# Performance work log

Measured on AMD Instinct MI355X. Metric: run time of the kernel, lower is better.

The kernel has to match this reference:

```python
import jax, jax.numpy as jnp
import numpy as np
from jax import lax

B, L, DIM = 2, 2048, 2048
HK, HV = 16, 32
DK, DV = 128, 128
KCONV = 4
KEY_DIM = HK * DK          # 2048
VAL_DIM = HV * DV          # 4096
CONV_DIM = 2 * KEY_DIM + VAL_DIM  # 8192
EPS = 1e-6


def _l2norm(x, eps=1e-6):
    return x * lax.rsqrt((x * x).sum(-1, keepdims=True) + eps)


def _gated_delta_rule(q, k, v, g, beta):
    # q,k: (B,L,H,DK); v: (B,L,H,DV); g,beta: (B,L,H)
    q = _l2norm(q.astype(jnp.float32)) * (DK ** -0.5)
    k = _l2norm(k.astype(jnp.float32))
    v = v.astype(jnp.float32)
    g = g.astype(jnp.float32)
    beta = beta.astype(jnp.float32)
    # time-major for scan: (L,B,H,...)
    qs = q.transpose(1, 0, 2, 3)
    ks = k.transpose(1, 0, 2, 3)
    vs = v.transpose(1, 0, 2, 3)
    gs = g.transpose(1, 0, 2)
    bs = beta.transpose(1, 0, 2)
    state0 = jnp.zeros((B, HV, DK, DV), jnp.float32)

    def step(state, inp):
        q_t, k_t, v_t, g_t, b_t = inp
        state = state * jnp.exp(g_t)[..., None, None]          # decay
        kv_mem = jnp.einsum('bhk,bhkv->bhv', k_t, state)       # read
        delta = (v_t - kv_mem) * b_t[..., None]                # error-correct
        state = state + jnp.einsum('bhk,bhv->bhkv', k_t, delta)
        out_t = jnp.einsum('bhk,bhkv->bhv', q_t, state)
        return state, out_t

    _, outs = lax.scan(step, state0, (qs, ks, vs, gs, bs))
    return outs.transpose(1, 0, 2, 3)  # (B,L,H,DV)


def setup_inputs() -> dict:
    key = jax.random.key(0)
    ks = jax.random.split(key, 8)
    s = 0.02
    return {
        'x': jax.random.normal(ks[0], (B, L, DIM), jnp.float32),
        'W_qkv': jax.random.normal(ks[1], (CONV_DIM, DIM), jnp.float32) * s,
        'W_z': jax.random.normal(ks[2], (VAL_DIM, DIM), jnp.float32) * s,
        'W_a': jax.random.normal(ks[3], (HV, DIM), jnp.float32) * s,
        'W_b': jax.random.normal(ks[4], (HV, DIM), jnp.float32) * s,
        'conv_w': jax.random.normal(ks[5], (CONV_DIM, 1, KCONV), jnp.float32) * 0.2,
        'A_log': jnp.log(jax.random.uniform(ks[6], (HV,), jnp.float32, 1e-6, 16.0)),
        'dt_bias': jnp.ones((HV,), jnp.float32),
        'norm_weight': jnp.ones((DV,), jnp.float32),
        'W_out': jax.random.normal(ks[7], (DIM, VAL_DIM), jnp.float32) * s,
    }


def reference(x, W_qkv, W_z, W_a, W_b, conv_w, A_log, dt_bias, norm_weight, W_out):
    qkv = x @ W_qkv.T                      # (B,L,CONV_DIM)
    z = x @ W_z.T                          # (B,L,VAL_DIM)
    a = x @ W_a.T                          # (B,L,HV)
    b = x @ W_b.T                          # (B,L,HV)
    # depthwise causal conv1d (left pad K-1)
    h = qkv.transpose(0, 2, 1)             # (B,C,L)
    h = lax.conv_general_dilated(h, conv_w, window_strides=(1,),
                                 padding=[(KCONV - 1, 0)],
                                 dimension_numbers=('NCH', 'OIH', 'NCH'),
                                 feature_group_count=CONV_DIM)
    qkv = jax.nn.silu(h.transpose(0, 2, 1))
    q, k, v = jnp.split(qkv, [KEY_DIM, 2 * KEY_DIM], axis=-1)
    q = q.reshape(B, L, HK, DK)
    k = k.reshape(B, L, HK, DK)
    v = v.reshape(B, L, HV, DV)
    rep = HV // HK
    if rep > 1:
        q = jnp.repeat(q, rep, axis=2)
        k = jnp.repeat(k, rep, axis=2)
    g = -jnp.exp(A_log.astype(jnp.float32)) * jax.nn.softplus(a.astype(jnp.float32) + dt_bias)
    beta = jax.nn.sigmoid(b)
    out = _gated_delta_rule(q, k, v, g, beta)   # (B,L,HV,DV) fp32
    # gated RMSNorm over DV: silu(z) * weight * norm(out)
    var = (out * out).mean(-1, keepdims=True)
    out = out * lax.rsqrt(var + EPS) * norm_weight
    zg = z.reshape(B, L, HV, DV)
    out = out * jax.nn.silu(zg.astype(jnp.float32))
    out = out.astype(x.dtype).reshape(B, L, VAL_DIM)
    return out @ W_out.T
```

## Files before the change

kernel.cpp:

```cpp
#include <hip/hip_runtime.h>
#include <hip/hip_bf16.h>
#include <cstddef>
#include <cstdint>

constexpr int B = 2, L = 2048, DIM = 2048;
constexpr int HK = 16, HV = 32, DK = 128, DV = 128;
constexpr int KEY_DIM = HK * DK;
constexpr int VAL_DIM = HV * DV;
constexpr int CONV_DIM = 2 * KEY_DIM + VAL_DIM;
constexpr int NPROJ = CONV_DIM + VAL_DIM + HV + HV;
constexpr int NPAD  = ((NPROJ + 255) / 256) * 256;
constexpr size_t ROWS = (size_t)B * L;
constexpr float EPS = 1e-6f;
constexpr int CHUNK = 64, NCHUNK = L / CHUNK;
constexpr int NCH_TOT = B * HV * NCHUNK;
constexpr int CONV_LT = 8;
constexpr int CONV_TL = L / CONV_LT;

constexpr size_t OFF_QKV  = 0;
constexpr size_t OFF_Z    = OFF_QKV + ROWS * CONV_DIM * 2;
constexpr size_t OFF_A    = OFF_Z   + ROWS * VAL_DIM * 2;
constexpr size_t OFF_B    = OFF_A   + ROWS * HV * 4;
constexpr size_t OFF_G    = OFF_B   + ROWS * HV * 4;
constexpr size_t OFF_BETA = OFF_G   + ROWS * HV * 4;
constexpr size_t OFF_U    = OFF_BETA + ROWS * HV * 4;
constexpr size_t OFF_WQK  = OFF_U + (size_t)NCH_TOT * CHUNK * DV * 4;
constexpr size_t OFF_HALO = OFF_WQK + (size_t)NCH_TOT * CHUNK * CHUNK * 2;
constexpr size_t WS_NEED_BYTES = OFF_HALO + (size_t)3 * B * CONV_LT * CONV_DIM * 2;
constexpr size_t OFF_WCAT = OFF_U;
constexpr size_t OFF_XB   = OFF_WQK;
constexpr size_t OFF_WOB  = OFF_U;
static_assert((size_t)NPAD * DIM * 2 <= (size_t)NCH_TOT * CHUNK * DV * 4, "Wcat fits U");

__device__ __forceinline__ float bf2f(unsigned short u) {
    union { float f; uint32_t i; } c; c.i = ((uint32_t)u) << 16; return c.f;
}
__device__ __forceinline__ unsigned short f2bf(float f) {
    union { float f; uint32_t u; } c; c.f = f;
    uint32_t u = c.u + 0x7FFFu + ((c.u >> 16) & 1u);
    return (unsigned short)(u >> 16);
}
__device__ __forceinline__ uint32_t pk2(float a, float b) {
    return (uint32_t)f2bf(a) | ((uint32_t)f2bf(b) << 16);
}

typedef __attribute__((ext_vector_type(8))) short bfrag;
typedef __attribute__((ext_vector_type(4))) float ffrag;

__device__ __forceinline__ void gload16(const unsigned short* g, unsigned short* l) {
    __builtin_amdgcn_global_load_lds(
        (const __attribute__((address_space(1))) uint32_t*)g,
        (__attribute__((address_space(3))) uint32_t*)l, 16, 0, 0);
}

__device__ __forceinline__ const float* w_row_multi(int n, const float* Wq, const float* Wz,
                                                    const float* Wa, const float* Wb) {
    if (n < CONV_DIM)                return Wq + (size_t)n * DIM;
    if (n < CONV_DIM + VAL_DIM)      return Wz + (size_t)(n - CONV_DIM) * DIM;
    if (n < CONV_DIM + VAL_DIM + HV) return Wa + (size_t)(n - CONV_DIM - VAL_DIM) * DIM;
    return Wb + (size_t)(n - CONV_DIM - VAL_DIM - HV) * DIM;
}

__global__ __launch_bounds__(256) void cvt_wcat(
    const float* __restrict__ Wq, const float* __restrict__ Wz,
    const float* __restrict__ Wa, const float* __restrict__ Wb,
    unsigned short* __restrict__ dst)
{
    const int r = blockIdx.x;
    const int c = threadIdx.x * 8;
    uint4 o;
    if (r < NPROJ) {
        const float* s = w_row_multi(r, Wq, Wz, Wa, Wb) + c;
        float4 v0 = *(const float4*)s;
        float4 v1 = *(const float4*)(s + 4);
        o = make_uint4(pk2(v0.x, v0.y), pk2(v0.z, v0.w), pk2(v1.x, v1.y), pk2(v1.z, v1.w));
    } else {
        o = make_uint4(0u, 0u, 0u, 0u);
    }
    *(uint4*)&dst[(size_t)r * DIM + c] = o;
}

__global__ __launch_bounds__(256) void cvt_f32bf(const float* __restrict__ src,
                                                 unsigned short* __restrict__ dst, int cols)
{
    const size_t r = blockIdx.x;
    for (int c = threadIdx.x * 8; c < cols; c += 256 * 8) {
        const float* s = src + r * cols + c;
        float4 v0 = *(const float4*)s;
        float4 v1 = *(const float4*)(s + 4);
        *(uint4*)&dst[r * cols + c] =
            make_uint4(pk2(v0.x, v0.y), pk2(v0.z, v0.w), pk2(v1.x, v1.y), pk2(v1.z, v1.w));
    }
}

__device__ __forceinline__ void store_multi(int m, int n, float v,
                                            unsigned short* qkv, unsigned short* z,
                                            float* a, float* b) {
    if (n < CONV_DIM) {
        qkv[(size_t)m * CONV_DIM + n] = f2bf(v);
    } else if (n < CONV_DIM + VAL_DIM) {
        z[(size_t)m * VAL_DIM + (n - CONV_DIM)] = f2bf(v);
    } else if (n < CONV_DIM + VAL_DIM + HV) {
        a[(size_t)m * HV + (n - CONV_DIM - VAL_DIM)] = v;
    } else if (n < NPROJ) {
        b[(size_t)m * HV + (n - CONV_DIM - VAL_DIM - HV)] = v;
    }
}

constexpr int BK = 64;

constexpr int GBUF = 24576;
constexpr int GEMM_SMEM = 3 * GBUF * 2;

__global__ __launch_bounds__(512, 1) void gemm_inproj_bf(
    const unsigned short* __restrict__ xb,
    const unsigned short* __restrict__ Wcat,
    unsigned short* __restrict__ qkv, unsigned short* __restrict__ z,
    float* __restrict__ a_out, float* __restrict__ b_out)
{
    extern __shared__ __align__(16) unsigned short lds[];

    constexpr int NT  = DIM / BK;
    constexpr int NBY = (int)ROWS / 256;
    constexpr int NBX = NPAD / 128;
    constexpr int NB  = NBY * NBX;
    const int id  = blockIdx.x;
    const int swz = (id & 7) * (NB >> 3) + (id >> 3);
    const int by  = swz & 15;
    const int bx  = swz >> 4;
    const int row0 = by * 256;
    const int col0 = bx * 128;

    const int t = threadIdx.x, lane = t & 63, wid = t >> 6;
    const int wr = wid >> 1, wc = wid & 1;
    const int quad = lane >> 4, l16 = lane & 15;
    const int x7 = l16 & 7;

    ffrag acc[4][4];
#pragma unroll
    for (int i = 0; i < 4; ++i)
#pragma unroll
        for (int j = 0; j < 4; ++j) acc[i][j] = (ffrag)0.f;

    const int srow = t >> 3;
    const int scol = (((t & 7) ^ (srow & 7)) * 8);
    const unsigned short* aS = xb   + (size_t)(row0 + srow) * DIM + scol;
    const unsigned short* bS = Wcat + (size_t)(col0 + srow) * DIM + scol;
    unsigned short* aD0 = lds + (wid * 8) * 64;
    unsigned short* bD0 = lds + 16384 + (wid * 8) * 64;

    auto STAGE = [&](int kt) {
        const int b = kt % 3;
        unsigned short* aD = aD0 + b * GBUF;
        unsigned short* bD = bD0 + b * GBUF;
        const int k0 = kt * BK;
#pragma unroll
        for (int g = 0; g < 4; ++g)
            gload16(aS + (size_t)(g * 64) * DIM + k0, aD + g * 64 * 64);
#pragma unroll
        for (int g = 0; g < 2; ++g)
            gload16(bS + (size_t)(g * 64) * DIM + k0, bD + g * 64 * 64);
    };

    auto COMPUTE = [&](int kt) {
        const int b = kt % 3;
        const unsigned short* A  = lds + b * GBUF;
        const unsigned short* Bm = lds + b * GBUF + 16384;
#pragma unroll
        for (int kk = 0; kk < 2; ++kk) {
            const int so = ((kk * 4 + quad) ^ x7) * 8;
            bfrag aF[4], bF[4];
#pragma unroll
            for (int m = 0; m < 4; ++m)
                aF[m] = *(const bfrag*)&A[(wr * 64 + m * 16 + l16) * 64 + so];
#pragma unroll
            for (int n = 0; n < 4; ++n)
                bF[n] = *(const bfrag*)&Bm[(wc * 64 + n * 16 + l16) * 64 + so];
#pragma unroll
            for (int m = 0; m < 4; ++m)
#pragma unroll
                for (int n = 0; n < 4; ++n)
                    acc[m][n] = __builtin_amdgcn_mfma_f32_16x16x32_bf16(
                        aF[m], bF[n], acc[m][n], 0, 0, 0);
        }
    };

    STAGE(0); STAGE(1);
    asm volatile("s_waitcnt vmcnt(6)" ::: "memory");
    asm volatile("s_barrier" ::: "memory");
    for (int kt = 0; kt < NT; ++kt) {
        if (kt + 2 < NT) {
            STAGE(kt + 2);
            asm volatile("s_waitcnt vmcnt(12)" ::: "memory");
        } else if (kt + 1 < NT) {
            asm volatile("s_waitcnt vmcnt(6)" ::: "memory");
        } else {
            asm volatile("s_waitcnt vmcnt(0)" ::: "memory");
        }
        asm volatile("s_barrier" ::: "memory");
        COMPUTE(kt);
        asm volatile("s_barrier" ::: "memory");
    }

#pragma unroll
    for (int m = 0; m < 4; ++m)
#pragma unroll
        for (int n = 0; n < 4; ++n) {
            int gr = row0 + wr * 64 + m * 16 + quad * 4;
            int gc = col0 + wc * 64 + n * 16 + l16;
#pragma unroll
            for (int reg = 0; reg < 4; ++reg)
                store_multi(gr + reg, gc, acc[m][n][reg], qkv, z, a_out, b_out);
        }
}

__global__ __launch_bounds__(512, 1) void gemm_outproj_bf(
    const unsigned short* __restrict__ A,
    const unsigned short* __restrict__ Wb,
    float* __restrict__ C)
{
    extern __shared__ __align__(16) unsigned short lds[];

    constexpr int NT  = VAL_DIM / BK;
    constexpr int NBY = (int)ROWS / 256;
    constexpr int NBX = DIM / 128;
    constexpr int NB  = NBY * NBX;
    const int id  = blockIdx.x;
    const int swz = (id & 7) * (NB >> 3) + (id >> 3);
    const int by  = swz & 15;
    const int bx  = swz >> 4;
    const int row0 = by * 256;
    const int col0 = bx * 128;

    const int t = threadIdx.x, lane = t & 63, wid = t >> 6;
    const int wr = wid >> 1, wc = wid & 1;
    const int quad = lane >> 4, l16 = lane & 15;
    const int x7 = l16 & 7;

    ffrag acc[4][4];
#pragma unroll
    for (int i = 0; i < 4; ++i)
#pragma unroll
        for (int j = 0; j < 4; ++j) acc[i][j] = (ffrag)0.f;

    const int srow = t >> 3;
    const int scol = (((t & 7) ^ (srow & 7)) * 8);
    const unsigned short* aS = A  + (size_t)(row0 + srow) * VAL_DIM + scol;
    const unsigned short* bS = Wb + (size_t)(col0 + srow) * VAL_DIM + scol;
    unsigned short* aD0 = lds + (wid * 8) * 64;
    unsigned short* bD0 = lds + 16384 + (wid * 8) * 64;

    auto STAGE = [&](int kt) {
        const int b = kt % 3;
        unsigned short* aD = aD0 + b * GBUF;
        unsigned short* bD = bD0 + b * GBUF;
        const int k0 = kt * BK;
#pragma unroll
        for (int g = 0; g < 4; ++g)
            gload16(aS + (size_t)(g * 64) * VAL_DIM + k0, aD + g * 64 * 64);
#pragma unroll
        for (int g = 0; g < 2; ++g)
            gload16(bS + (size_t)(g * 64) * VAL_DIM + k0, bD + g * 64 * 64);
    };

    auto COMPUTE = [&](int kt) {
        const int b = kt % 3;
        const unsigned short* Am = lds + b * GBUF;
        const unsigned short* Bm = lds + b * GBUF + 16384;
#pragma unroll
        for (int kk = 0; kk < 2; ++kk) {
            const int so = ((kk * 4 + quad) ^ x7) * 8;
            bfrag aF[4], bF[4];
#pragma unroll
            for (int m = 0; m < 4; ++m)
                aF[m] = *(const bfrag*)&Am[(wr * 64 + m * 16 + l16) * 64 + so];
#pragma unroll
            for (int n = 0; n < 4; ++n)
                bF[n] = *(const bfrag*)&Bm[(wc * 64 + n * 16 + l16) * 64 + so];
#pragma unroll
            for (int m = 0; m < 4; ++m)
#pragma unroll
                for (int n = 0; n < 4; ++n)
                    acc[m][n] = __builtin_amdgcn_mfma_f32_16x16x32_bf16(
                        aF[m], bF[n], acc[m][n], 0, 0, 0);
        }
    };

    STAGE(0); STAGE(1);
    asm volatile("s_waitcnt vmcnt(6)" ::: "memory");
    asm volatile("s_barrier" ::: "memory");
    for (int kt = 0; kt < NT; ++kt) {
        if (kt + 2 < NT) {
            STAGE(kt + 2);
            asm volatile("s_waitcnt vmcnt(12)" ::: "memory");
        } else if (kt + 1 < NT) {
            asm volatile("s_waitcnt vmcnt(6)" ::: "memory");
        } else {
            asm volatile("s_waitcnt vmcnt(0)" ::: "memory");
        }
        asm volatile("s_barrier" ::: "memory");
        COMPUTE(kt);
        asm volatile("s_barrier" ::: "memory");
    }

#pragma unroll
    for (int m = 0; m < 4; ++m)
#pragma unroll
        for (int n = 0; n < 4; ++n) {
            int gr = row0 + wr * 64 + m * 16 + quad * 4;
            int gc = col0 + wc * 64 + n * 16 + l16;
#pragma unroll
            for (int reg = 0; reg < 4; ++reg)
                C[(size_t)(gr + reg) * DIM + gc] = acc[m][n][reg];
        }
}

__global__ __launch_bounds__(256) void conv_halo(const unsigned short* __restrict__ qkv,
                                                 unsigned short* __restrict__ hbuf)
{
    int idx = blockIdx.x * 256 + threadIdx.x;
    int c    = idx & (CONV_DIM - 1);
    int tile = (idx >> 13) & (CONV_LT - 1);
    int b    = idx >> 16;
    int l0 = tile * CONV_TL;
    const unsigned short* p = qkv + (size_t)b * L * CONV_DIM + c;
#pragma unroll
    for (int j = 0; j < 3; ++j) {
        unsigned short v = (tile > 0) ? p[(size_t)(l0 - 3 + j) * CONV_DIM] : (unsigned short)0;
        hbuf[((size_t)j * B * CONV_LT + b * CONV_LT + tile) * CONV_DIM + c] = v;
    }
}

__global__ __launch_bounds__(256) void conv_silu(unsigned short* __restrict__ qkv,
                                                 const float* __restrict__ conv_w,
                                                 const unsigned short* __restrict__ hbuf)
{
    int idx = blockIdx.x * 256 + threadIdx.x;
    int c    = idx & (CONV_DIM - 1);
    int tile = (idx >> 13) & (CONV_LT - 1);
    int b    = idx >> 16;
    const float w0 = conv_w[c * 4 + 0];
    const float w1 = conv_w[c * 4 + 1];
    const float w2 = conv_w[c * 4 + 2];
    const float w3 = conv_w[c * 4 + 3];
    unsigned short* p = qkv + ((size_t)b * L + tile * CONV_TL) * CONV_DIM + c;
    const size_t hb = (size_t)b * CONV_LT + tile;
    float x0 = bf2f(hbuf[((size_t)0 * B * CONV_LT + hb) * CONV_DIM + c]);
    float x1 = bf2f(hbuf[((size_t)1 * B * CONV_LT + hb) * CONV_DIM + c]);
    float x2 = bf2f(hbuf[((size_t)2 * B * CONV_LT + hb) * CONV_DIM + c]);
    for (int l0 = 0; l0 < CONV_TL; l0 += 8) {
        float xv[8];
#pragma unroll
        for (int j = 0; j < 8; ++j) xv[j] = bf2f(p[(size_t)(l0 + j) * CONV_DIM]);
#pragma unroll
        for (int j = 0; j < 8; ++j) {
            float h = w0 * x0 + w1 * x1 + w2 * x2 + w3 * xv[j];
            float s = h / (1.f + __expf(-h));
            p[(size_t)(l0 + j) * CONV_DIM] = f2bf(s);
            x0 = x1; x1 = x2; x2 = xv[j];
        }
    }
}

__global__ __launch_bounds__(256) void normqk(unsigned short* __restrict__ qkv)
{
    int wid  = blockIdx.x * 4 + (threadIdx.x >> 6);
    int lane = threadIdx.x & 63;
    int hk  = wid & 15;
    int sel = (wid >> 4) & 1;
    int row = wid >> 5;
    unsigned short* p = qkv + (size_t)row * CONV_DIM + sel * KEY_DIM + hk * DK;
    float x0 = bf2f(p[lane]), x1 = bf2f(p[lane + 64]);
    float ss = x0 * x0 + x1 * x1;
#pragma unroll
    for (int o = 32; o >= 1; o >>= 1) ss += __shfl_xor(ss, o);
    float sc = rsqrtf(ss + 1e-6f);
    if (sel == 0) sc *= 0.08838834764831845f;
    p[lane]      = f2bf(x0 * sc);
    p[lane + 64] = f2bf(x1 * sc);
}

__global__ __launch_bounds__(256) void gatecoef(const float* __restrict__ a_buf,
                                                const float* __restrict__ b_buf,
                                                const float* __restrict__ A_log,
                                                const float* __restrict__ dt_bias,
                                                float* __restrict__ glog,
                                                float* __restrict__ beta)
{
    int idx = blockIdx.x * blockDim.x + threadIdx.x;
    int h = idx & (HV - 1);
    float av = a_buf[idx];
    float bv = b_buf[idx];
    float x  = av + dt_bias[h];
    float sp = (x > 20.f) ? x : log1pf(__expf(x));
    glog[idx] = -__expf(A_log[h]) * sp;
    beta[idx] = 1.f / (1.f + __expf(-bv));
}


constexpr int RSK  = 136;
constexpr int RST  = 72;
constexpr int RSTD = 68;
constexpr int RSR1 = 260;

constexpr int P1_oKs  = 0;
constexpr int P1_oQs  = P1_oKs + 64 * RSK * 2;
constexpr int P1_oDT  = 0;
constexpr int P1_oAf  = P1_oQs + 64 * RSK * 2;
constexpr int P1_oRHS = P1_oAf + 64 * RST * 2;
constexpr int P1_oG   = P1_oRHS + 64 * RSR1 * 4;
constexpr int P1_oEG  = P1_oG + 256;
constexpr int P1_oBs  = P1_oEG + 256;
constexpr int P1_SMEM = P1_oBs + 256;

__global__ __launch_bounds__(256, 1) void chunk_prep(
    unsigned short* __restrict__ qkv,
    const float* __restrict__ glog,
    const float* __restrict__ beta,
    float* __restrict__ Ubuf,
    unsigned short* __restrict__ Wqkbuf)
{
    extern __shared__ __align__(16) char smem[];
    unsigned short* sKs = (unsigned short*)(smem + P1_oKs);
    unsigned short* sQs = (unsigned short*)(smem + P1_oQs);
    unsigned short* sDT = (unsigned short*)(smem + P1_oDT);
    unsigned short* sAf = (unsigned short*)(smem + P1_oAf);
    float* sRHS = (float*)(smem + P1_oRHS);
    float* sG   = (float*)(smem + P1_oG);
    float* sEG  = (float*)(smem + P1_oEG);
    float* sBs  = (float*)(smem + P1_oBs);

    const int bid = blockIdx.x;
    const int ch = bid & (NCHUNK - 1);
    const int h  = (bid >> 5) & (HV - 1);
    const int bb = bid >> 10;
    const int hk = h >> 1;
    const int t    = threadIdx.x;
    const int w    = t >> 6;
    const int lane = t & 63;
    const int quad = lane >> 4;
    const int l16  = lane & 15;
    const int quad8 = quad * 8;
    const size_t bL = (size_t)bb * L;
    const int l0 = ch * CHUNK;
    const int VOFF = 2 * KEY_DIM + h * DV;

    {
        const int r  = t >> 2;
        const int c0 = (t & 3) * 32;
        const unsigned short* grow = qkv + (bL + l0 + r) * CONV_DIM;
        const unsigned short* gq = grow + hk * DK + c0;
        const unsigned short* gk = grow + KEY_DIM + hk * DK + c0;
#pragma unroll
        for (int u = 0; u < 4; ++u) {
            *(uint4*)&sKs[r * RSK + c0 + 8 * u] = *(const uint4*)(gk + 8 * u);
            *(uint4*)&sQs[r * RSK + c0 + 8 * u] = *(const uint4*)(gq + 8 * u);
        }
        if (t < 64) {
            float gl = glog[(bL + l0 + t) * HV + h];
#pragma unroll
            for (int off = 1; off < 64; off <<= 1) {
                float v = __shfl_up(gl, off, 64);
                if (lane >= off) gl += v;
            }
            sG[t]  = gl;
            sEG[t] = __expf(gl);
            sBs[t] = beta[(bL + l0 + t) * HV + h];
        }
    }
    __syncthreads();

    {
        ffrag accA[4], accW[4];
#pragma unroll
        for (int mt = 0; mt < 4; ++mt) { accA[mt] = (ffrag)0.f; accW[mt] = (ffrag)0.f; }
#pragma unroll
        for (int kk = 0; kk < 4; ++kk) {
            bfrag bf = *(const bfrag*)&sKs[(16 * w + l16) * RSK + 32 * kk + quad8];
#pragma unroll
            for (int mt = 0; mt < 4; ++mt) {
                bfrag ak = *(const bfrag*)&sKs[(16 * mt + l16) * RSK + 32 * kk + quad8];
                bfrag aq = *(const bfrag*)&sQs[(16 * mt + l16) * RSK + 32 * kk + quad8];
                accA[mt] = __builtin_amdgcn_mfma_f32_16x16x32_bf16(ak, bf, accA[mt], 0, 0, 0);
                accW[mt] = __builtin_amdgcn_mfma_f32_16x16x32_bf16(aq, bf, accW[mt], 0, 0, 0);
            }
        }
        const int j = 16 * w + l16;
        const float gj = sG[j];
        unsigned short* Wqp = Wqkbuf + (size_t)bid * (CHUNK * CHUNK);
#pragma unroll
        for (int mt = 0; mt < 4; ++mt)
#pragma unroll
            for (int reg = 0; reg < 4; ++reg) {
                int i = 16 * mt + quad * 4 + reg;
                float sc = __expf(sG[i] - gj);
                sAf[i * RST + j] = f2bf((j < i) ? sBs[i] * sc * accA[mt][reg] : 0.f);
                Wqp[i * CHUNK + j] = f2bf((j <= i) ? sc * accW[mt][reg] : 0.f);
            }
    }

    {
        const int r  = t >> 2;
        const int c0 = (t & 3) * 32;
        const float be  = sBs[r];
        const float beg = be * sEG[r];
        const unsigned short* gv = qkv + (bL + l0 + r) * CONV_DIM + VOFF + c0;
#pragma unroll
        for (int u = 0; u < 4; ++u) {
            uint4 vv = *(const uint4*)(gv + 8 * u);
            const unsigned short* vp = (const unsigned short*)&vv;
#pragma unroll
            for (int e = 0; e < 8; ++e)
                sRHS[r * RSR1 + c0 + 8 * u + e] = be * bf2f(vp[e]);
        }
#pragma unroll
        for (int u = 0; u < 4; ++u)
#pragma unroll
            for (int e = 0; e < 8; ++e)
                sRHS[r * RSR1 + 128 + c0 + 8 * u + e] =
                    beg * bf2f(sKs[r * RSK + c0 + 8 * u + e]);
    }
    __syncthreads();

    for (int u = t; u < 256 * RSTD / 2; u += 256) ((uint32_t*)sDT)[u] = 0;

    float* Up = Ubuf + (size_t)bid * (CHUNK * DV);
    for (int sb = 0; sb < 4; ++sb) {
        const int sb16 = 16 * sb;
        if (sb > 0) {
            const int kbn = (sb + 1) >> 1;
            ffrag c16[4];
#pragma unroll
            for (int nt = 0; nt < 4; ++nt) c16[nt] = (ffrag)0.f;
            for (int kb = 0; kb < kbn; ++kb) {
                bfrag af = *(const bfrag*)&sAf[(sb16 + l16) * RST + 32 * kb + quad8];
#pragma unroll
                for (int nt = 0; nt < 4; ++nt) {
                    bfrag bf = *(const bfrag*)&sDT[(64 * w + 16 * nt + l16) * RSTD + 32 * kb + quad8];
                    c16[nt] = __builtin_amdgcn_mfma_f32_16x16x32_bf16(af, bf, c16[nt], 0, 0, 0);
                }
            }
#pragma unroll
            for (int nt = 0; nt < 4; ++nt)
#pragma unroll
                for (int reg = 0; reg < 4; ++reg)
                    sRHS[(sb16 + quad * 4 + reg) * RSR1 + 64 * w + 16 * nt + l16] -= c16[nt][reg];
        }
        __syncthreads();
        {
            const int c = t;
            float d16[16];
#pragma unroll
            for (int e = 0; e < 16; ++e) {
                const int i = sb16 + e;
                float acc = sRHS[i * RSR1 + c];
#pragma unroll
                for (int f = 0; f < 16; ++f)
                    if (f < e) acc -= bf2f(sAf[i * RST + sb16 + f]) * d16[f];
                d16[e] = acc;
            }
#pragma unroll
            for (int e = 0; e < 16; e += 2)
                *(uint32_t*)&sDT[c * RSTD + sb16 + e] = pk2(d16[e], d16[e + 1]);
            if (c < 128) {
                float* up = Up + c;
#pragma unroll
                for (int e = 0; e < 16; ++e) up[(size_t)(sb16 + e) * DV] = d16[e];
            } else {
                unsigned short* wp = qkv + (bL + l0 + sb16) * CONV_DIM + VOFF + (c - 128);
#pragma unroll
                for (int e = 0; e < 16; ++e) wp[(size_t)e * CONV_DIM] = f2bf(-d16[e]);
            }
        }
        __syncthreads();
    }
}

constexpr int P2_oSTb = 0;
constexpr int P2_oWk  = P2_oSTb + 128 * RSK * 2;
constexpr int P2_oQs  = P2_oWk + 64 * RSK * 2;
constexpr int P2_oKT  = P2_oQs + 64 * RSK * 2;
constexpr int P2_oWqk = P2_oKT + 128 * RST * 2;
constexpr int P2_oDT  = P2_oWqk + 64 * RST * 2;
constexpr int P2_oDdT = P2_oDT + 128 * RST * 2;
constexpr int P2_oEG  = P2_oDdT + 128 * RST * 2;
constexpr int P2_oEGd = P2_oEG + 256;
constexpr int P2_oNW  = P2_oEGd + 256;
constexpr int P2_oP   = P2_oNW + 512;
constexpr int P2_SMEM = P2_oP + 512;

__global__ __launch_bounds__(512, 1) void chunk_scan2(
    const unsigned short* __restrict__ qkv,
    const float* __restrict__ glog,
    const float* __restrict__ Ubuf,
    const unsigned short* __restrict__ Wqkbuf,
    unsigned short* __restrict__ z_io,
    const float* __restrict__ norm_w)
{
    extern __shared__ __align__(16) char smem[];
    unsigned short* sSTb = (unsigned short*)(smem + P2_oSTb);
    unsigned short* sWk  = (unsigned short*)(smem + P2_oWk);
    unsigned short* sQs  = (unsigned short*)(smem + P2_oQs);
    unsigned short* sKT  = (unsigned short*)(smem + P2_oKT);
    unsigned short* sWqk = (unsigned short*)(smem + P2_oWqk);
    unsigned short* sDT  = (unsigned short*)(smem + P2_oDT);
    unsigned short* sDdT = (unsigned short*)(smem + P2_oDdT);
    float* sEG  = (float*)(smem + P2_oEG);
    float* sEGd = (float*)(smem + P2_oEGd);
    float* sNW  = (float*)(smem + P2_oNW);
    float* sP   = (float*)(smem + P2_oP);

    const int bb = blockIdx.x >> 5;
    const int h  = blockIdx.x & (HV - 1);
    const int hk = h >> 1;
    const int t    = threadIdx.x;
    const int w    = t >> 6;
    const int lane = t & 63;
    const int quad = lane >> 4;
    const int l16  = lane & 15;
    const int quad8 = quad * 8;
    const int rg = w >> 1;
    const int dh = w & 1;
    const size_t bL = (size_t)bb * L;
    const int VOFF = 2 * KEY_DIM + h * DV;
    const size_t chbase0 = ((size_t)bb * HV + h) * NCHUNK;

    const int r  = t >> 3;
    const int c0 = (t & 7) * 16;
    const int cw = (t & 7) * 8;

    ffrag accS[8];
#pragma unroll
    for (int nt = 0; nt < 8; ++nt) accS[nt] = (ffrag)0.f;

    for (int u = t; u < 64 * RSK; u += 512) ((uint32_t*)sSTb)[u] = 0;
    if (t < 128) sNW[t] = norm_w[t];

    uint4 pQ[2], pK[2], pWk[2], pWqk;
    float pGl;

    auto PF = [&](int ch) {
        const int l0p = ch * CHUNK;
        const unsigned short* grow = qkv + (bL + l0p + r) * CONV_DIM;
        const unsigned short* gq = grow + hk * DK + c0;
        const unsigned short* gk = grow + KEY_DIM + hk * DK + c0;
        const unsigned short* gw = grow + VOFF + c0;
#pragma unroll
        for (int u = 0; u < 2; ++u) {
            pQ[u]  = *(const uint4*)(gq + 8 * u);
            pK[u]  = *(const uint4*)(gk + 8 * u);
            pWk[u] = *(const uint4*)(gw + 8 * u);
        }
        pWqk = *(const uint4*)(Wqkbuf + (chbase0 + ch) * (CHUNK * CHUNK) + r * CHUNK + cw);
        pGl = glog[(bL + l0p + (t & 63)) * HV + h];
    };

    PF(0);

    for (int ch = 0; ch < NCHUNK; ++ch) {
        const int l0 = ch * CHUNK;
        const size_t cb = chbase0 + ch;
        __syncthreads();

        ffrag accD[4];
        {
            const float* up = Ubuf + cb * (CHUNK * DV) + (size_t)(quad * 4) * DV + 16 * w + l16;
#pragma unroll
            for (int mt = 0; mt < 4; ++mt)
#pragma unroll
                for (int reg = 0; reg < 4; ++reg)
                    accD[mt][reg] = up[(size_t)(16 * mt + reg) * DV];
        }
        unsigned short pz[4][4];
        {
            const unsigned short* zp =
                z_io + (bL + l0 + 16 * rg + quad * 4) * (size_t)VAL_DIM + h * DV + 64 * dh + l16;
#pragma unroll
            for (int nt = 0; nt < 4; ++nt)
#pragma unroll
                for (int reg = 0; reg < 4; ++reg)
                    pz[nt][reg] = zp[(size_t)reg * VAL_DIM + 16 * nt];
        }

#pragma unroll
        for (int u = 0; u < 2; ++u) {
            *(uint4*)&sQs[r * RSK + c0 + 8 * u] = pQ[u];
            *(uint4*)&sWk[r * RSK + c0 + 8 * u] = pWk[u];
            const unsigned short* kp = (const unsigned short*)&pK[u];
#pragma unroll
            for (int e = 0; e < 8; ++e) {
                const int c = c0 + 8 * u + e;
                sKT[c * RST + ((((r >> 3) ^ (c >> 3)) & 7) << 3) + (r & 7)] = kp[e];
            }
        }
        *(uint4*)&sWqk[r * RST + cw] = pWqk;

        {
            float gl = pGl;
            if (t < 64) {
#pragma unroll
                for (int off = 1; off < 64; off <<= 1) {
                    float v = __shfl_up(gl, off, 64);
                    if (lane >= off) gl += v;
                }
                float gc = __shfl(gl, 63, 64);
                sEG[t]  = __expf(gl);
                sEGd[t] = __expf(gc - gl);
            }
        }

        if (ch + 1 < NCHUNK) PF(ch + 1);
        __syncthreads();

#pragma unroll
        for (int kk = 0; kk < 4; ++kk) {
            bfrag b0 = *(const bfrag*)&sSTb[(16 * w + l16) * RSK + 32 * kk + quad8];
#pragma unroll
            for (int mt = 0; mt < 4; ++mt) {
                bfrag af = *(const bfrag*)&sWk[(16 * mt + l16) * RSK + 32 * kk + quad8];
                accD[mt] = __builtin_amdgcn_mfma_f32_16x16x32_bf16(af, b0, accD[mt], 0, 0, 0);
            }
        }

        {
            const int dv = 16 * w + l16;
#pragma unroll
            for (int mt = 0; mt < 4; ++mt) {
                const int i0 = 16 * mt + quad * 4;
                const float e0 = sEGd[i0], e1 = sEGd[i0 + 1], e2 = sEGd[i0 + 2], e3 = sEGd[i0 + 3];
                const float d0 = accD[mt][0], d1 = accD[mt][1];
                const float d2 = accD[mt][2], d3 = accD[mt][3];
                *(uint32_t*)&sDT[dv * RST + i0]      = pk2(d0, d1);
                *(uint32_t*)&sDT[dv * RST + i0 + 2]  = pk2(d2, d3);
                *(uint32_t*)&sDdT[dv * RST + i0]     = pk2(d0 * e0, d1 * e1);
                *(uint32_t*)&sDdT[dv * RST + i0 + 2] = pk2(d2 * e2, d3 * e3);
            }
        }
        __syncthreads();

        ffrag accO[4];
#pragma unroll
        for (int nt = 0; nt < 4; ++nt) accO[nt] = (ffrag)0.f;
#pragma unroll
        for (int kk = 0; kk < 4; ++kk) {
            bfrag af = *(const bfrag*)&sQs[(16 * rg + l16) * RSK + 32 * kk + quad8];
#pragma unroll
            for (int nt = 0; nt < 4; ++nt) {
                bfrag bf = *(const bfrag*)&sSTb[(64 * dh + 16 * nt + l16) * RSK + 32 * kk + quad8];
                accO[nt] = __builtin_amdgcn_mfma_f32_16x16x32_bf16(af, bf, accO[nt], 0, 0, 0);
            }
        }
#pragma unroll
        for (int nt = 0; nt < 4; ++nt)
#pragma unroll
            for (int reg = 0; reg < 4; ++reg)
                accO[nt][reg] *= sEG[16 * rg + quad * 4 + reg];
#pragma unroll
        for (int kk = 0; kk < 2; ++kk) {
            bfrag af = *(const bfrag*)&sWqk[(16 * rg + l16) * RST + 32 * kk + quad8];
#pragma unroll
            for (int nt = 0; nt < 4; ++nt) {
                bfrag bf = *(const bfrag*)&sDT[(64 * dh + 16 * nt + l16) * RST + 32 * kk + quad8];
                accO[nt] = __builtin_amdgcn_mfma_f32_16x16x32_bf16(af, bf, accO[nt], 0, 0, 0);
            }
        }

        float p4[4];
#pragma unroll
        for (int reg = 0; reg < 4; ++reg) {
            float p = 0.f;
#pragma unroll
            for (int nt = 0; nt < 4; ++nt) p += accO[nt][reg] * accO[nt][reg];
#pragma unroll
            for (int m = 1; m < 16; m <<= 1) p += __shfl_xor(p, m, 64);
            p4[reg] = p;
        }
        if (l16 == 0) {
#pragma unroll
            for (int reg = 0; reg < 4; ++reg) sP[w * 16 + quad * 4 + reg] = p4[reg];
        }

        {
            const float eGc = sEG[63];
#pragma unroll
            for (int nt = 0; nt < 8; ++nt)
#pragma unroll
                for (int reg = 0; reg < 4; ++reg) accS[nt][reg] *= eGc;
#pragma unroll
            for (int kk = 0; kk < 2; ++kk) {
                bfrag a0 = *(const bfrag*)&sDdT[(16 * w + l16) * RST + 32 * kk + quad8];
#pragma unroll
                for (int nt = 0; nt < 8; ++nt) {
                    const int ck = 16 * nt + l16;
                    bfrag bk = *(const bfrag*)&sKT[ck * RST +
                                 ((((4 * kk + quad) ^ (ck >> 3)) & 7) << 3)];
                    accS[nt] = __builtin_amdgcn_mfma_f32_16x16x32_bf16(a0, bk, accS[nt], 0, 0, 0);
                }
            }
        }
        __syncthreads();

        {
            float inv[4];
#pragma unroll
            for (int reg = 0; reg < 4; ++reg) {
                float pp = p4[reg] + sP[(w ^ 1) * 16 + quad * 4 + reg];
                inv[reg] = rsqrtf(pp * (1.f / 128.f) + EPS);
            }
            unsigned short* zw =
                z_io + (bL + l0 + 16 * rg + quad * 4) * (size_t)VAL_DIM + h * DV + 64 * dh + l16;
#pragma unroll
            for (int nt = 0; nt < 4; ++nt) {
                const float nwv = sNW[64 * dh + 16 * nt + l16];
#pragma unroll
                for (int reg = 0; reg < 4; ++reg) {
                    float zv = bf2f(pz[nt][reg]);
                    float y = accO[nt][reg] * inv[reg] * nwv * (zv / (1.f + __expf(-zv)));
                    zw[(size_t)reg * VAL_DIM + 16 * nt] = f2bf(y);
                }
            }
        }

#pragma unroll
        for (int nt = 0; nt < 8; ++nt)
#pragma unroll
            for (int reg = 0; reg < 4; ++reg)
                sSTb[(16 * w + quad * 4 + reg) * RSK + 16 * nt + l16] = f2bf(accS[nt][reg]);
    }
}

extern "C" void kernel_launch(void* const* d_in, const int* in_sizes, int n_in,
                              void* d_out, int out_size, void* d_ws, size_t ws_size,
                              hipStream_t stream)
{
    const float* x        = (const float*)d_in[0];
    const float* W_qkv    = (const float*)d_in[1];
    const float* W_z      = (const float*)d_in[2];
    const float* W_a      = (const float*)d_in[3];
    const float* W_b      = (const float*)d_in[4];
    const float* conv_w   = (const float*)d_in[5];
    const float* A_log    = (const float*)d_in[6];
    const float* dt_bias  = (const float*)d_in[7];
    const float* norm_w   = (const float*)d_in[8];
    const float* W_out    = (const float*)d_in[9];
    float* out = (float*)d_out;
    char*  ws  = (char*)d_ws;

    if (ws_size < WS_NEED_BYTES) return;

    unsigned short* qkv = (unsigned short*)(ws + OFF_QKV);
    unsigned short* z   = (unsigned short*)(ws + OFF_Z);
    float* a    = (float*)(ws + OFF_A);
    float* bbuf = (float*)(ws + OFF_B);
    float* gl   = (float*)(ws + OFF_G);
    float* beta = (float*)(ws + OFF_BETA);
    float* Ubuf = (float*)(ws + OFF_U);
    unsigned short* Wqkbuf = (unsigned short*)(ws + OFF_WQK);
    unsigned short* hbuf   = (unsigned short*)(ws + OFF_HALO);
    unsigned short* Wcat   = (unsigned short*)(ws + OFF_WCAT);
    unsigned short* xb     = (unsigned short*)(ws + OFF_XB);
    unsigned short* Wob    = (unsigned short*)(ws + OFF_WOB);

    static bool attr_set = false;
    if (!attr_set) {
        (void)hipFuncSetAttribute((const void*)chunk_prep,
                                  hipFuncAttributeMaxDynamicSharedMemorySize, P1_SMEM);
        (void)hipFuncSetAttribute((const void*)chunk_scan2,
                                  hipFuncAttributeMaxDynamicSharedMemorySize, P2_SMEM);
        (void)hipFuncSetAttribute((const void*)gemm_inproj_bf,
                                  hipFuncAttributeMaxDynamicSharedMemorySize, GEMM_SMEM);
        (void)hipFuncSetAttribute((const void*)gemm_outproj_bf,
                                  hipFuncAttributeMaxDynamicSharedMemorySize, GEMM_SMEM);
        attr_set = true;
    }

    cvt_wcat<<<NPAD, 256, 0, stream>>>(W_qkv, W_z, W_a, W_b, Wcat);
    cvt_f32bf<<<(int)ROWS, 256, 0, stream>>>(x, xb, DIM);
    gemm_inproj_bf<<<((int)ROWS / 256) * (NPAD / 128), 512, GEMM_SMEM, stream>>>(
        xb, Wcat, qkv, z, a, bbuf);
    conv_halo<<<(B * CONV_LT * CONV_DIM) / 256, 256, 0, stream>>>(qkv, hbuf);
    conv_silu<<<(B * CONV_LT * CONV_DIM) / 256, 256, 0, stream>>>(qkv, conv_w, hbuf);
    normqk<<<(B * L * 2 * HK) / 4, 256, 0, stream>>>(qkv);
    gatecoef<<<(B * L * HV) / 256, 256, 0, stream>>>(a, bbuf, A_log, dt_bias, gl, beta);
    chunk_prep<<<NCH_TOT, 256, P1_SMEM, stream>>>(qkv, gl, beta, Ubuf, Wqkbuf);
    chunk_scan2<<<B * HV, 512, P2_SMEM, stream>>>(qkv, gl, Ubuf, Wqkbuf, z, norm_w);
    cvt_f32bf<<<DIM, 256, 0, stream>>>(W_out, Wob, VAL_DIM);
    gemm_outproj_bf<<<((int)ROWS / 256) * (DIM / 128), 512, GEMM_SMEM, stream>>>(z, Wob, out);
}
```

Before: 924.8 us.

## Retile projection GEMMs to 128x128 with 4 waves, double buffering, and finer conv tiles

Both projection GEMMs now use 128x128 output tiles with 256 threads instead of 256x128 with 512 threads. The triple-buffered LDS ring is replaced by a double buffer that is issued right after each compute step, and the MFMA block is wrapped in raised wave priority. LDS use and block size both shrink, so more blocks can fit per CU and the larger grid should help latency hiding, at the cost of less operand reuse per tile. The causal conv is also split into 16 sequence tiles instead of 8 for more parallelism, with its index math and halo size adjusted to match.

```diff
diff --git a/kernel.cpp b/kernel.cpp
--- a/kernel.cpp
+++ b/kernel.cpp
@@ -14,7 +14,7 @@
 constexpr float EPS = 1e-6f;
 constexpr int CHUNK = 64, NCHUNK = L / CHUNK;
 constexpr int NCH_TOT = B * HV * NCHUNK;
-constexpr int CONV_LT = 8;
+constexpr int CONV_LT = 16;
 constexpr int CONV_TL = L / CONV_LT;
 
 constexpr size_t OFF_QKV  = 0;
@@ -109,10 +109,10 @@
 
 constexpr int BK = 64;
 
-constexpr int GBUF = 24576;
-constexpr int GEMM_SMEM = 3 * GBUF * 2;
-
-__global__ __launch_bounds__(512, 1) void gemm_inproj_bf(
+constexpr int GBUF2 = 16384;
+constexpr int GEMM_SMEM = 2 * GBUF2 * 2;
+
+__global__ __launch_bounds__(256) void gemm_inproj_bf(
     const unsigned short* __restrict__ xb,
     const unsigned short* __restrict__ Wcat,
     unsigned short* __restrict__ qkv, unsigned short* __restrict__ z,
@@ -121,18 +121,18 @@
     extern __shared__ __align__(16) unsigned short lds[];
 
     constexpr int NT  = DIM / BK;
-    constexpr int NBY = (int)ROWS / 256;
+    constexpr int NBY = (int)ROWS / 128;
     constexpr int NBX = NPAD / 128;
     constexpr int NB  = NBY * NBX;
     const int id  = blockIdx.x;
     const int swz = (id & 7) * (NB >> 3) + (id >> 3);
-    const int by  = swz & 15;
-    const int bx  = swz >> 4;
-    const int row0 = by * 256;
+    const int by  = swz & 31;
+    const int bx  = swz >> 5;
+    const int row0 = by * 128;
     const int col0 = bx * 128;
 
     const int t = threadIdx.x, lane = t & 63, wid = t >> 6;
-    const int wr = wid >> 1, wc = wid & 1;
+    const int wm = (wid >> 1) * 64, wn = (wid & 1) * 64;
     const int quad = lane >> 4, l16 = lane & 15;
     const int x7 = l16 & 7;
 
@@ -147,74 +147,74 @@
     const unsigned short* aS = xb   + (size_t)(row0 + srow) * DIM + scol;
     const unsigned short* bS = Wcat + (size_t)(col0 + srow) * DIM + scol;
     unsigned short* aD0 = lds + (wid * 8) * 64;
-    unsigned short* bD0 = lds + 16384 + (wid * 8) * 64;
+    unsigned short* bD0 = lds + 8192 + (wid * 8) * 64;
 
     auto STAGE = [&](int kt) {
-        const int b = kt % 3;
-        unsigned short* aD = aD0 + b * GBUF;
-        unsigned short* bD = bD0 + b * GBUF;
+        const int b = kt & 1;
+        unsigned short* aD = aD0 + b * GBUF2;
+        unsigned short* bD = bD0 + b * GBUF2;
         const int k0 = kt * BK;
 #pragma unroll
-        for (int g = 0; g < 4; ++g)
-            gload16(aS + (size_t)(g * 64) * DIM + k0, aD + g * 64 * 64);
-#pragma unroll
-        for (int g = 0; g < 2; ++g)
-            gload16(bS + (size_t)(g * 64) * DIM + k0, bD + g * 64 * 64);
+        for (int g = 0; g < 4; ++g) {
+            gload16(aS + (size_t)(g * 32) * DIM + k0, aD + g * 32 * 64);
+            gload16(bS + (size_t)(g * 32) * DIM + k0, bD + g * 32 * 64);
+        }
     };
 
     auto COMPUTE = [&](int kt) {
-        const int b = kt % 3;
-        const unsigned short* A  = lds + b * GBUF;
-        const unsigned short* Bm = lds + b * GBUF + 16384;
+        const int b = kt & 1;
+        const unsigned short* A  = lds + b * GBUF2;
+        const unsigned short* Bm = lds + b * GBUF2 + 8192;
 #pragma unroll
         for (int kk = 0; kk < 2; ++kk) {
             const int so = ((kk * 4 + quad) ^ x7) * 8;
             bfrag aF[4], bF[4];
 #pragma unroll
             for (int m = 0; m < 4; ++m)
-                aF[m] = *(const bfrag*)&A[(wr * 64 + m * 16 + l16) * 64 + so];
+                aF[m] = *(const bfrag*)&A[(wm + m * 16 + l16) * 64 + so];
 #pragma unroll
             for (int n = 0; n < 4; ++n)
-                bF[n] = *(const bfrag*)&Bm[(wc * 64 + n * 16 + l16) * 64 + so];
+                bF[n] = *(const bfrag*)&Bm[(wn + n * 16 + l16) * 64 + so];
+            __builtin_amdgcn_s_setprio(1);
 #pragma unroll
             for (int m = 0; m < 4; ++m)
 #pragma unroll
                 for (int n = 0; n < 4; ++n)
                     acc[m][n] = __builtin_amdgcn_mfma_f32_16x16x32_bf16(
                         aF[m], bF[n], acc[m][n], 0, 0, 0);
+            __builtin_amdgcn_s_setprio(0);
         }
     };
 
     STAGE(0); STAGE(1);
-    asm volatile("s_waitcnt vmcnt(6)" ::: "memory");
+    asm volatile("s_waitcnt vmcnt(8)" ::: "memory");
     asm volatile("s_barrier" ::: "memory");
     for (int kt = 0; kt < NT; ++kt) {
+        COMPUTE(kt);
+        if (kt == NT - 1) break;
+        asm volatile("s_barrier" ::: "memory");
         if (kt + 2 < NT) {
             STAGE(kt + 2);
-            asm volatile("s_waitcnt vmcnt(12)" ::: "memory");
-        } else if (kt + 1 < NT) {
-            asm volatile("s_waitcnt vmcnt(6)" ::: "memory");
+            asm volatile("s_waitcnt vmcnt(8)" ::: "memory");
         } else {
             asm volatile("s_waitcnt vmcnt(0)" ::: "memory");
         }
         asm volatile("s_barrier" ::: "memory");
-        COMPUTE(kt);
-        asm volatile("s_barrier" ::: "memory");
     }
 
 #pragma unroll
     for (int m = 0; m < 4; ++m)
 #pragma unroll
         for (int n = 0; n < 4; ++n) {
-            int gr = row0 + wr * 64 + m * 16 + quad * 4;
-            int gc = col0 + wc * 64 + n * 16 + l16;
+            int gr = row0 + wm + m * 16 + quad * 4;
+            int gc = col0 + wn + n * 16 + l16;
 #pragma unroll
             for (int reg = 0; reg < 4; ++reg)
                 store_multi(gr + reg, gc, acc[m][n][reg], qkv, z, a_out, b_out);
         }
 }
 
-__global__ __launch_bounds__(512, 1) void gemm_outproj_bf(
+__global__ __launch_bounds__(256) void gemm_outproj_bf(
     const unsigned short* __restrict__ A,
     const unsigned short* __restrict__ Wb,
     float* __restrict__ C)
@@ -222,18 +222,18 @@
     extern __shared__ __align__(16) unsigned short lds[];
 
     constexpr int NT  = VAL_DIM / BK;
-    constexpr int NBY = (int)ROWS / 256;
+    constexpr int NBY = (int)ROWS / 128;
     constexpr int NBX = DIM / 128;
     constexpr int NB  = NBY * NBX;
     const int id  = blockIdx.x;
     const int swz = (id & 7) * (NB >> 3) + (id >> 3);
-    const int by  = swz & 15;
-    const int bx  = swz >> 4;
-    const int row0 = by * 256;
+    const int by  = swz & 31;
+    const int bx  = swz >> 5;
+    const int row0 = by * 128;
     const int col0 = bx * 128;
 
     const int t = threadIdx.x, lane = t & 63, wid = t >> 6;
-    const int wr = wid >> 1, wc = wid & 1;
+    const int wm = (wid >> 1) * 64, wn = (wid & 1) * 64;
     const int quad = lane >> 4, l16 = lane & 15;
     const int x7 = l16 & 7;
 
@@ -248,67 +248,67 @@
     const unsigned short* aS = A  + (size_t)(row0 + srow) * VAL_DIM + scol;
     const unsigned short* bS = Wb + (size_t)(col0 + srow) * VAL_DIM + scol;
     unsigned short* aD0 = lds + (wid * 8) * 64;
-    unsigned short* bD0 = lds + 16384 + (wid * 8) * 64;
+    unsigned short* bD0 = lds + 8192 + (wid * 8) * 64;
 
     auto STAGE = [&](int kt) {
-        const int b = kt % 3;
-        unsigned short* aD = aD0 + b * GBUF;
-        unsigned short* bD = bD0 + b * GBUF;
+        const int b = kt & 1;
+        unsigned short* aD = aD0 + b * GBUF2;
+        unsigned short* bD = bD0 + b * GBUF2;
         const int k0 = kt * BK;
 #pragma unroll
-        for (int g = 0; g < 4; ++g)
-            gload16(aS + (size_t)(g * 64) * VAL_DIM + k0, aD + g * 64 * 64);
-#pragma unroll
-        for (int g = 0; g < 2; ++g)
-            gload16(bS + (size_t)(g * 64) * VAL_DIM + k0, bD + g * 64 * 64);
+        for (int g = 0; g < 4; ++g) {
+            gload16(aS + (size_t)(g * 32) * VAL_DIM + k0, aD + g * 32 * 64);
+            gload16(bS + (size_t)(g * 32) * VAL_DIM + k0, bD + g * 32 * 64);
+        }
     };
 
     auto COMPUTE = [&](int kt) {
-        const int b = kt % 3;
-        const unsigned short* Am = lds + b * GBUF;
-        const unsigned short* Bm = lds + b * GBUF + 16384;
+        const int b = kt & 1;
+        const unsigned short* Am = lds + b * GBUF2;
+        const unsigned short* Bm = lds + b * GBUF2 + 8192;
 #pragma unroll
         for (int kk = 0; kk < 2; ++kk) {
             const int so = ((kk * 4 + quad) ^ x7) * 8;
             bfrag aF[4], bF[4];
 #pragma unroll
             for (int m = 0; m < 4; ++m)
-                aF[m] = *(const bfrag*)&Am[(wr * 64 + m * 16 + l16) * 64 + so];
+                aF[m] = *(const bfrag*)&Am[(wm + m * 16 + l16) * 64 + so];
 #pragma unroll
             for (int n = 0; n < 4; ++n)
-                bF[n] = *(const bfrag*)&Bm[(wc * 64 + n * 16 + l16) * 64 + so];
+                bF[n] = *(const bfrag*)&Bm[(wn + n * 16 + l16) * 64 + so];
+            __builtin_amdgcn_s_setprio(1);
 #pragma unroll
             for (int m = 0; m < 4; ++m)
 #pragma unroll
                 for (int n = 0; n < 4; ++n)
                     acc[m][n] = __builtin_amdgcn_mfma_f32_16x16x32_bf16(
                         aF[m], bF[n], acc[m][n], 0, 0, 0);
+            __builtin_amdgcn_s_setprio(0);
         }
     };
 
     STAGE(0); STAGE(1);
-    asm volatile("s_waitcnt vmcnt(6)" ::: "memory");
+    asm volatile("s_waitcnt vmcnt(8)" ::: "memory");
     asm volatile("s_barrier" ::: "memory");
     for (int kt = 0; kt < NT; ++kt) {
+        COMPUTE(kt);
+        if (kt == NT - 1) break;
+        asm volatile("s_barrier" ::: "memory");
         if (kt + 2 < NT) {
             STAGE(kt + 2);
-            asm volatile("s_waitcnt vmcnt(12)" ::: "memory");
-        } else if (kt + 1 < NT) {
-            asm volatile("s_waitcnt vmcnt(6)" ::: "memory");
+            asm volatile("s_waitcnt vmcnt(8)" ::: "memory");
         } else {
             asm volatile("s_waitcnt vmcnt(0)" ::: "memory");
         }
         asm volatile("s_barrier" ::: "memory");
-        COMPUTE(kt);
-        asm volatile("s_barrier" ::: "memory");
     }
 
 #pragma unroll
     for (int m = 0; m < 4; ++m)
 #pragma unroll
         for (int n = 0; n < 4; ++n) {
-            int gr = row0 + wr * 64 + m * 16 + quad * 4;
-            int gc = col0 + wc * 64 + n * 16 + l16;
+            int gr = row0 + wm + m * 16 + quad * 4;
+            int gc = col0 + wn + n * 16 + l16;
 #pragma unroll
             for (int reg = 0; reg < 4; ++reg)
                 C[(size_t)(gr + reg) * DIM + gc] = acc[m][n][reg];
@@ -321,7 +321,7 @@
     int idx = blockIdx.x * 256 + threadIdx.x;
     int c    = idx & (CONV_DIM - 1);
     int tile = (idx >> 13) & (CONV_LT - 1);
-    int b    = idx >> 16;
+    int b    = idx >> 17;
     int l0 = tile * CONV_TL;
     const unsigned short* p = qkv + (size_t)b * L * CONV_DIM + c;
 #pragma unroll
@@ -338,7 +338,7 @@
     int idx = blockIdx.x * 256 + threadIdx.x;
     int c    = idx & (CONV_DIM - 1);
     int tile = (idx >> 13) & (CONV_LT - 1);
-    int b    = idx >> 16;
+    int b    = idx >> 17;
     const float w0 = conv_w[c * 4 + 0];
     const float w1 = conv_w[c * 4 + 1];
     const float w2 = conv_w[c * 4 + 2];
@@ -876,7 +876,7 @@
 
     cvt_wcat<<<NPAD, 256, 0, stream>>>(W_qkv, W_z, W_a, W_b, Wcat);
     cvt_f32bf<<<(int)ROWS, 256, 0, stream>>>(x, xb, DIM);
-    gemm_inproj_bf<<<((int)ROWS / 256) * (NPAD / 128), 512, GEMM_SMEM, stream>>>(
+    gemm_inproj_bf<<<((int)ROWS / 128) * (NPAD / 128), 256, GEMM_SMEM, stream>>>(
         xb, Wcat, qkv, z, a, bbuf);
     conv_halo<<<(B * CONV_LT * CONV_DIM) / 256, 256, 0, stream>>>(qkv, hbuf);
     conv_silu<<<(B * CONV_LT * CONV_DIM) / 256, 256, 0, stream>>>(qkv, conv_w, hbuf);
@@ -885,5 +885,5 @@
     chunk_prep<<<NCH_TOT, 256, P1_SMEM, stream>>>(qkv, gl, beta, Ubuf, Wqkbuf);
     chunk_scan2<<<B * HV, 512, P2_SMEM, stream>>>(qkv, gl, Ubuf, Wqkbuf, z, norm_w);
     cvt_f32bf<<<DIM, 256, 0, stream>>>(W_out, Wob, VAL_DIM);
-    gemm_outproj_bf<<<((int)ROWS / 256) * (DIM / 128), 512, GEMM_SMEM, stream>>>(z, Wob, out);
-}
+    gemm_outproj_bf<<<((int)ROWS / 128) * (DIM / 128), 256, GEMM_SMEM, stream>>>(z, Wob, out);
+}
```

Result: no change. 937.0 us (+1.3%).
